# Kernel optimization log

Hardware: AMD Instinct MI355X
Metric: run time of the kernel (lower is better)

## Reference

```python
import jax, jax.numpy as jnp
import numpy as np

NS, NV = 48, 10
N_NODES, N_EDGES = 10000, 100000
N_EDGE_FEAT = 3 * NS  # 144
W_SS, W_VS, W_SV, W_VV = NS * NS, NV * NS, NS * NV, NV * NV
W_NUMEL = W_SS + W_VS + W_SV + W_VV  # 3364 = FullyConnectedTensorProduct.weight_numel
IN_DIM = NS + 3 * NV  # 78
EPS = 1e-5


def setup_inputs() -> dict:
    key = jax.random.key(0)
    ks = jax.random.split(key, 8)
    return {
        "node_attr": jax.random.normal(ks[0], (N_NODES, IN_DIM), jnp.float32),
        "edge_attr": jax.random.normal(ks[1], (N_EDGES, N_EDGE_FEAT), jnp.float32),
        "edge_sh": jax.random.normal(ks[2], (N_EDGES, 4), jnp.float32),
        "fc1_w": jax.random.normal(ks[3], (N_EDGE_FEAT, N_EDGE_FEAT), jnp.float32) / np.sqrt(N_EDGE_FEAT).astype(np.float32),
        "fc1_b": jnp.zeros((N_EDGE_FEAT,), jnp.float32),
        "fc2_w": jax.random.normal(ks[4], (N_EDGE_FEAT, W_NUMEL), jnp.float32) / np.sqrt(N_EDGE_FEAT).astype(np.float32),
        "fc2_b": jnp.zeros((W_NUMEL,), jnp.float32),
        "bn_weight": jnp.ones((NS + NV,), jnp.float32),
        "bn_bias": jnp.zeros((NS,), jnp.float32),
        "edge_index": jax.random.randint(ks[5], (2, N_EDGES), 0, N_NODES),
    }


def reference(node_attr, edge_attr, edge_sh, fc1_w, fc1_b, fc2_w, fc2_b, bn_weight, bn_bias, edge_index):
    edge_src, edge_dst = edge_index[0], edge_index[1]
    # --- gather node feats per edge, split into irreps ---
    x = node_attr[edge_dst]                      # [E, 78]
    xs = x[:, :NS]                               # [E, 48]  scalars (0e)
    xv = x[:, NS:].reshape(-1, NV, 3)            # [E, 10, 3] vectors (1o)
    s0 = edge_sh[:, 0]                           # [E]     sh 0e
    s1 = edge_sh[:, 1:4]                         # [E, 3]  sh 1o

    # --- per-edge TP weights from edge MLP ---
    w = jax.nn.relu(edge_attr @ fc1_w + fc1_b) @ fc2_w + fc2_b  # [E, 3364]
    w_ss = w[:, :W_SS].reshape(-1, NS, NS)
    w_vs = w[:, W_SS:W_SS + W_VS].reshape(-1, NV, NS)
    w_sv = w[:, W_SS + W_VS:W_SS + W_VS + W_SV].reshape(-1, NS, NV)
    w_vv = w[:, W_SS + W_VS + W_SV:].reshape(-1, NV, NV)

    # path normalization: 1/sqrt(mul_in * n_paths_into_output_irrep)
    a_ss = 1.0 / np.sqrt(NS * 2.0)
    a_vs = 1.0 / np.sqrt(NV * 2.0)
    a_sv = 1.0 / np.sqrt(NS * 2.0)
    a_vv = 1.0 / np.sqrt(NV * 2.0)

    # --- Clebsch-Gordan tensor product (fully connected, per-edge weights) ---
    # 0e (x) 0e -> 0e
    out_s = a_ss * jnp.einsum('ei,eio->eo', xs, w_ss) * s0[:, None]
    # 1o (x) 1o -> 0e  (CG = delta/sqrt(3))
    dot = jnp.einsum('eic,ec->ei', xv, s1) / np.sqrt(3.0)
    out_s = out_s + a_vs * jnp.einsum('ei,eio->eo', dot, w_vs)
    # 0e (x) 1o -> 1o
    out_v = a_sv * jnp.einsum('ei,eio->eo', xs, w_sv)[:, :, None] * s1[:, None, :]
    # 1o (x) 0e -> 1o
    out_v = out_v + a_vv * jnp.einsum('eic,eio->eoc', xv, w_vv) * s0[:, None, None]

    tp = jnp.concatenate([out_s, out_v.reshape(-1, 3 * NV)], axis=1)  # [E, 78]

    # --- scatter-mean to nodes ---
    sums = jax.ops.segment_sum(tp, edge_src, num_segments=N_NODES)
    cnt = jax.ops.segment_sum(jnp.ones((tp.shape[0],), tp.dtype), edge_src, num_segments=N_NODES)
    out = sums / jnp.maximum(cnt, 1.0)[:, None]

    # --- residual (in_dim == out_dim -> pad is a no-op) ---
    out = out + node_attr

    # --- equivariant batch norm (e3nn-style, batch statistics) ---
    os = out[:, :NS]
    ov = out[:, NS:].reshape(-1, NV, 3)
    mu = os.mean(0)
    var = os.var(0)
    os = (os - mu) / jnp.sqrt(var + EPS) * bn_weight[:NS] + bn_bias
    fn = (ov ** 2).sum(-1).mean(0) / 3.0  # component-normalized mean squared norm per channel
    ov = ov / jnp.sqrt(fn + EPS)[None, :, None] * bn_weight[NS:][None, :, None]
    return jnp.concatenate([os, ov.reshape(-1, 3 * NV)], axis=1)
```

## Files before the change

### kernel.cpp

```cpp
#include <hip/hip_runtime.h>
#include <hip/hip_bf16.h>

#define NS   48
#define NV   10
#define NEF  144
#define WN   3364
#define IND  78
#define NE   100000
#define NN   10000
#define EPS  1e-5f
#define HP   144

#define A_SS 0.10206207261596575f
#define A_VS 0.22360679774997896f
#define A_SV 0.10206207261596575f
#define A_VV 0.22360679774997896f
#define RS3  0.5773502691896258f

typedef __attribute__((ext_vector_type(8)))  short  short8;
typedef __attribute__((ext_vector_type(16))) float  f32x16;
typedef __attribute__((ext_vector_type(4)))  int    int4v;
typedef __attribute__((ext_vector_type(4)))  float  float4v;
typedef __attribute__((ext_vector_type(2)))  float  float2v;

#define MFMA32(a,b,c) __builtin_amdgcn_mfma_f32_32x32x16_bf16((a),(b),(c),0,0,0)

#define TP_F    0
#define ST_F    7800000
#define CNT_F   7800160
#define OFFS_F  7810160
#define CUR_F   7820164
#define EL_F    7830164
#define WSBF_F  7930168

#define OFF_W1  0
#define OFF_B1  23040
#define OFF_B2  468480
#define OFF_B3  561664
#define N_PREP  608256

__device__ __forceinline__ short tobf(float v) {
    return __builtin_bit_cast(short, __float2bfloat16(v));
}
__device__ __forceinline__ float fromb(short s) {
    unsigned u = ((unsigned)(unsigned short)s) << 16;
    return __builtin_bit_cast(float, u);
}
__device__ __forceinline__ unsigned pkt2(float a, float b) {
    unsigned ua = __builtin_bit_cast(unsigned, a);
    unsigned ub = __builtin_bit_cast(unsigned, b);
    return (ua >> 16) | (ub & 0xFFFF0000u);
}
__device__ __forceinline__ float waveReduceSum(float v) {
    #pragma unroll
    for (int o = 32; o > 0; o >>= 1) v += __shfl_down(v, o, 64);
    return v;
}

__global__ void prep_weights(const float* __restrict__ fc1_w,
                             const float* __restrict__ fc2_w,
                             const float* __restrict__ b2,
                             short* __restrict__ wsbf)
{
    int idx = blockIdx.x * 256 + threadIdx.x;
    if (idx >= N_PREP) return;
    float v = 0.f;
    if (idx < OFF_B1) {
        int r = idx;
        int tile = r / 4608, rem = r % 4608;
        int ks = rem / 512, l = (rem % 512) / 8, j = rem % 8;
        int n = tile * 32 + (l & 31);
        int k = ks * 16 + ((l >> 5) << 3) + j;
        v = (n < 144) ? fc1_w[k * 144 + n] : 0.f;
    } else if (idx < OFF_B2) {
        int r = idx - OFF_B1;
        if (r < 442368) {
            int i = r / 9216, rem = r % 9216;
            int tile = rem / 4608; rem %= 4608;
            int ks = rem / 512, l = (rem % 512) / 8, j = rem % 8;
            int n = tile * 32 + (l & 31);
            int k = ks * 16 + ((l >> 5) << 3) + j;
            if (n < 48)      v = fc2_w[(size_t)k * WN + i * 48 + n];
            else if (n < 58) v = fc2_w[(size_t)k * WN + 2784 + i * 10 + (n - 48)];
        } else {
            int rb = r - 442368;
            int tile = rb / 1536, rem = rb % 1536;
            int ks = rem / 512, l = (rem % 512) / 8, j = rem % 8;
            int n = tile * 32 + (l & 31);
            int k = ks * 16 + ((l >> 5) << 3) + j;
            if (n < 48)      v = b2[k * 48 + n];
            else if (n < 58) v = b2[2784 + k * 10 + (n - 48)];
        }
    } else if (idx < OFF_B3) {
        int r = idx - OFF_B2;
        if (r < 92160) {
            int i = r / 9216, rem = r % 9216;
            int tile = rem / 4608; rem %= 4608;
            int ks = rem / 512, l = (rem % 512) / 8, j = rem % 8;
            int n = tile * 32 + (l & 31);
            int k = ks * 16 + ((l >> 5) << 3) + j;
            if (n < 48) v = fc2_w[(size_t)k * WN + 2304 + i * 48 + n];
        } else {
            int rb = r - 92160;
            int tile = rb / 512, rem = rb % 512;
            int l = rem / 8, j = rem % 8;
            int n = tile * 32 + (l & 31);
            int k = ((l >> 5) << 3) + j;
            if (k < 10 && n < 48) v = b2[2304 + k * 48 + n];
        }
    } else {
        int r = idx - OFF_B3;
        if (r < 46080) {
            int i = r / 4608, rem = r % 4608;
            int ks = rem / 512, l = (rem % 512) / 8, j = rem % 8;
            int n = l & 31;
            int k = ks * 16 + ((l >> 5) << 3) + j;
            if (n < 10) v = fc2_w[(size_t)k * WN + 3264 + i * 10 + n];
        } else {
            int rb = r - 46080;
            int l = rb / 8, j = rb % 8;
            int n = l & 31;
            int k = ((l >> 5) << 3) + j;
            if (k < 10 && n < 10) v = b2[3264 + k * 10 + n];
        }
    }
    wsbf[idx] = tobf(v);
}

__global__ void hist_kernel(const int* __restrict__ eidx, int* __restrict__ cntI)
{
    int e = blockIdx.x * 256 + threadIdx.x;
    if (e < NE) atomicAdd(&cntI[eidx[e]], 1);
}

__global__ __launch_bounds__(1024) void scan_kernel(const int* __restrict__ cntI,
                                                    int* __restrict__ offs,
                                                    int* __restrict__ cursor)
{
    __shared__ int part[1024];
    int t = threadIdx.x;
    int base = t * 10;
    int local[10];
    int s = 0;
    #pragma unroll
    for (int q = 0; q < 10; ++q) {
        int i = base + q;
        int v = (i < NN) ? cntI[i] : 0;
        local[q] = s; s += v;
    }
    part[t] = s;
    __syncthreads();
    for (int o = 1; o < 1024; o <<= 1) {
        int v = (t >= o) ? part[t - o] : 0;
        __syncthreads();
        part[t] += v;
        __syncthreads();
    }
    int prev = (t == 0) ? 0 : part[t - 1];
    #pragma unroll
    for (int q = 0; q < 10; ++q) {
        int i = base + q;
        if (i < NN) { int val = prev + local[q]; offs[i] = val; cursor[i] = val; }
    }
    if (t == 1023) offs[NN] = part[1023];
}

__global__ void scatter_kernel(const int* __restrict__ eidx,
                               int* __restrict__ cursor, int* __restrict__ elist)
{
    int e = blockIdx.x * 256 + threadIdx.x;
    if (e < NE) {
        int pos = atomicAdd(&cursor[eidx[e]], 1);
        elist[pos] = e;
    }
}

__global__ __launch_bounds__(128, 2) void fused_main(
    const float* __restrict__ node_attr, const float* __restrict__ edge_attr,
    const float* __restrict__ edge_sh,   const float* __restrict__ b1,
    const int*   __restrict__ eidx,      const short* __restrict__ wsbf,
    float* __restrict__ tp)
{
    __shared__ short hlds[64 * HP];
    __shared__ short xfT[96 * 64];
    __shared__ float pbuf[64][10];
    __shared__ float s0s[64];
    __shared__ float s1s[64][3];

    const int t    = threadIdx.x;
    const int e0   = blockIdx.x * 64;
    const int lane = t & 63, wave = t >> 6;
    const int n32  = lane & 31, kh = lane >> 5;
    const int eL   = 32 * wave + n32;
    const int eLc  = min(e0 + eL, NE - 1);

    const short* W1L = wsbf + OFF_W1 + lane * 8;
    const short* B1L = wsbf + OFF_B1 + lane * 8;
    const short* B2L = wsbf + OFF_B2 + lane * 8;
    const short* B3L = wsbf + OFF_B3 + lane * 8;

    for (int idx = t; idx < 8 * 64; idx += 128) xfT[88 * 64 + idx] = 0;

    if (t < 64) {
        int ee = e0 + t;
        if (ee < NE) {
            float4v sh = *reinterpret_cast<const float4v*>(edge_sh + (size_t)ee * 4);
            s0s[t] = sh.x; s1s[t][0] = sh.y; s1s[t][1] = sh.z; s1s[t][2] = sh.w;
        } else {
            s0s[t] = 0.f; s1s[t][0] = s1s[t][1] = s1s[t][2] = 0.f;
        }
    }

    {
        const int eg  = t & 63;
        const int jb  = t >> 6;
        const int egc = min(e0 + eg, NE - 1);
        const int dst = eidx[NE + egc];
        const float* na = node_attr + (size_t)dst * IND;
        for (int j = jb; j < IND; j += 2) {
            int slot = (j < NS) ? j : 58 + ((j - NS) % 3) * 10 + (j - NS) / 3;
            xfT[slot * 64 + eg] = tobf(na[j]);
        }
    }

    short8 afc[9];
    {
        const float* ea = edge_attr + (size_t)eLc * NEF + kh * 8;
        #pragma unroll
        for (int ks = 0; ks < 9; ++ks) {
            float4v lo = *reinterpret_cast<const float4v*>(ea + ks * 16);
            float4v hi = *reinterpret_cast<const float4v*>(ea + ks * 16 + 4);
            int4v v = { (int)pkt2(lo.x, lo.y), (int)pkt2(lo.z, lo.w),
                        (int)pkt2(hi.x, hi.y), (int)pkt2(hi.z, hi.w) };
            afc[ks] = __builtin_bit_cast(short8, v);
        }
    }
    __syncthreads();

    #pragma unroll
    for (int it = 0; it < 5; ++it) {
        int e = t & 63;
        int i = (t >> 6) + 2 * it;
        float d = fromb(xfT[(58 + i) * 64 + e]) * s1s[e][0]
                + fromb(xfT[(68 + i) * 64 + e]) * s1s[e][1]
                + fromb(xfT[(78 + i) * 64 + e]) * s1s[e][2];
        xfT[(48 + i) * 64 + e] = tobf(d * RS3);
    }

    for (int pass = 0; pass < 3; ++pass) {
        int ntA = 2 * pass, ntB = 2 * pass + 1;
        bool hasB = (pass < 2);
        f32x16 accA = 0, accB = 0;
        #pragma unroll
        for (int ks = 0; ks < 9; ++ks) {
            short8 bA = *(const short8*)(W1L + (ntA * 9 + ks) * 512);
            accA = MFMA32(afc[ks], bA, accA);
            if (hasB) {
                short8 bB = *(const short8*)(W1L + (ntB * 9 + ks) * 512);
                accB = MFMA32(afc[ks], bB, accB);
            }
        }
        int colA = ntA * 32 + n32, colB = ntB * 32 + n32;
        float b1A = (colA < NEF) ? b1[colA] : 0.f;
        float b1B = (hasB && colB < NEF) ? b1[colB] : 0.f;
        #pragma unroll
        for (int r = 0; r < 16; ++r) {
            int row = (r & 3) + 8 * (r >> 2) + 4 * kh;
            int e = 32 * wave + row;
            if (colA < NEF) hlds[e * HP + colA] = tobf(fmaxf(accA[r] + b1A, 0.f));
            if (hasB)       hlds[e * HP + colB] = tobf(fmaxf(accB[r] + b1B, 0.f));
        }
    }
    __syncthreads();

    float2v hreg[36];
    #pragma unroll
    for (int ks = 0; ks < 9; ++ks) {
        int4v hh = *(const int4v*)(hlds + eL * HP + ks * 16 + kh * 8);
        #pragma unroll
        for (int q = 0; q < 4; ++q) {
            unsigned u = (unsigned)hh[q];
            float2v p;
            p.x = __builtin_bit_cast(float, u << 16);
            p.y = __builtin_bit_cast(float, u & 0xFFFF0000u);
            hreg[ks * 4 + q] = p;
        }
    }

    const int eoff = eL;

    f32x16 acc1a = 0, acc1b = 0, acc2a = 0, acc2b = 0;
    {
        #pragma unroll 1
        for (int i = 0; i < 48; ++i) {
            float xv = fromb(xfT[i * 64 + eoff]);
            float2v x2; x2.x = xv; x2.y = xv;
            const short* p0 = B1L + i * 9216;
            #pragma unroll
            for (int ks = 0; ks < 9; ++ks) {
                int4v v;
                #pragma unroll
                for (int q = 0; q < 4; ++q) {
                    float2v pr = hreg[ks * 4 + q] * x2;
                    v[q] = (int)pkt2(pr.x, pr.y);
                }
                short8 a  = __builtin_bit_cast(short8, v);
                short8 b0 = *(const short8*)(p0 + ks * 512);
                short8 b1f= *(const short8*)(p0 + 4608 + ks * 512);
                acc1a = MFMA32(a, b0, acc1a);
                acc1b = MFMA32(a, b1f, acc1b);
            }
        }
        #pragma unroll
        for (int ks = 0; ks < 3; ++ks) {
            short8 a;
            #pragma unroll
            for (int j = 0; j < 8; ++j)
                a[j] = xfT[(ks * 16 + kh * 8 + j) * 64 + eoff];
            short8 b0 = *(const short8*)(B1L + 442368 + ks * 512);
            short8 b1f= *(const short8*)(B1L + 442368 + 1536 + ks * 512);
            acc1a = MFMA32(a, b0, acc1a);
            acc1b = MFMA32(a, b1f, acc1b);
        }
    }
    {
        #pragma unroll 1
        for (int i = 0; i < 10; ++i) {
            float xv = fromb(xfT[(48 + i) * 64 + eoff]);
            float2v x2; x2.x = xv; x2.y = xv;
            const short* p0 = B2L + i * 9216;
            #pragma unroll
            for (int ks = 0; ks < 9; ++ks) {
                int4v v;
                #pragma unroll
                for (int q = 0; q < 4; ++q) {
                    float2v pr = hreg[ks * 4 + q] * x2;
                    v[q] = (int)pkt2(pr.x, pr.y);
                }
                short8 a  = __builtin_bit_cast(short8, v);
                short8 b0 = *(const short8*)(p0 + ks * 512);
                short8 b1f= *(const short8*)(p0 + 4608 + ks * 512);
                acc2a = MFMA32(a, b0, acc2a);
                acc2b = MFMA32(a, b1f, acc2b);
            }
        }
        {
            short8 a;
            #pragma unroll
            for (int j = 0; j < 8; ++j)
                a[j] = xfT[(48 + kh * 8 + j) * 64 + eoff];
            short8 b0 = *(const short8*)(B2L + 92160);
            short8 b1f= *(const short8*)(B2L + 92160 + 512);
            acc2a = MFMA32(a, b0, acc2a);
            acc2b = MFMA32(a, b1f, acc2b);
        }
    }
    #pragma unroll
    for (int r = 0; r < 16; ++r) {
        int row = (r & 3) + 8 * (r >> 2) + 4 * kh;
        int e = 32 * wave + row;
        int ge = e0 + e;
        if (ge < NE) {
            float s0e = s0s[e];
            float* rowp = tp + (size_t)ge * IND;
            rowp[n32] = A_SS * s0e * acc1a[r] + A_VS * acc2a[r];
            int col = 32 + n32;
            if (col < 48) {
                rowp[col] = A_SS * s0e * acc1b[r] + A_VS * acc2b[r];
            } else if (col < 58) {
                pbuf[e][col - 48] = A_SV * acc1b[r];
            }
        }
    }
    {
        #pragma unroll 1
        for (int c = 0; c < 3; ++c) {
            f32x16 acc3 = 0;
            #pragma unroll 1
            for (int i = 0; i < 10; ++i) {
                float xv = fromb(xfT[(58 + c * 10 + i) * 64 + eoff]);
                float2v x2; x2.x = xv; x2.y = xv;
                const short* p0 = B3L + i * 4608;
                #pragma unroll
                for (int ks = 0; ks < 9; ++ks) {
                    int4v v;
                    #pragma unroll
                    for (int q = 0; q < 4; ++q) {
                        float2v pr = hreg[ks * 4 + q] * x2;
                        v[q] = (int)pkt2(pr.x, pr.y);
                    }
                    short8 a  = __builtin_bit_cast(short8, v);
                    short8 b0 = *(const short8*)(p0 + ks * 512);
                    acc3 = MFMA32(a, b0, acc3);
                }
            }
            {
                short8 a;
                #pragma unroll
                for (int j = 0; j < 8; ++j)
                    a[j] = xfT[(58 + c * 10 + kh * 8 + j) * 64 + eoff];
                short8 b0 = *(const short8*)(B3L + 46080);
                acc3 = MFMA32(a, b0, acc3);
            }
            if (n32 < 10) {
                #pragma unroll
                for (int r = 0; r < 16; ++r) {
                    int row = (r & 3) + 8 * (r >> 2) + 4 * kh;
                    int e = 32 * wave + row;
                    int ge = e0 + e;
                    if (ge < NE) {
                        float p = pbuf[e][n32];
                        float q = A_VV * s0s[e] * acc3[r];
                        tp[(size_t)ge * IND + 48 + n32 * 3 + c] = p * s1s[e][c] + q;
                    }
                }
            }
        }
    }
}

__global__ __launch_bounds__(256) void gather_kernel(const float* __restrict__ tp,
                                                     const int* __restrict__ offs,
                                                     const int* __restrict__ elist,
                                                     const float* __restrict__ node_attr,
                                                     float* __restrict__ out)
{
    int node = blockIdx.x * 4 + (threadIdx.x >> 6);
    int lane = threadIdx.x & 63;
    if (node >= NN) return;
    int beg = offs[node], end = offs[node + 1];
    float a0 = 0.f, a1 = 0.f;
    for (int p = beg; p < end; ++p) {
        int e = elist[p];
        const float* row = tp + (size_t)e * IND;
        a0 += row[lane];
        if (lane < 14) a1 += row[64 + lane];
    }
    float c = fmaxf((float)(end - beg), 1.0f);
    size_t base = (size_t)node * IND;
    out[base + lane] = a0 / c + node_attr[base + lane];
    if (lane < 14) out[base + 64 + lane] = a1 / c + node_attr[base + 64 + lane];
}

__global__ __launch_bounds__(256) void stats_kernel(const float* __restrict__ pre,
                                                    const float* __restrict__ bnw,
                                                    float* __restrict__ stats)
{
    int j = blockIdx.x;
    int t = threadIdx.x;
    float s1 = 0.f, s2 = 0.f;
    if (j < NS) {
        for (int n = t; n < NN; n += 256) {
            float v = pre[(size_t)n * IND + j];
            s1 += v; s2 += v * v;
        }
    } else {
        int vch = j - NS;
        for (int n = t; n < NN; n += 256) {
            float a = pre[(size_t)n * IND + NS + vch * 3 + 0];
            float b = pre[(size_t)n * IND + NS + vch * 3 + 1];
            float d = pre[(size_t)n * IND + NS + vch * 3 + 2];
            s2 += a * a + b * b + d * d;
        }
    }
    __shared__ float r1[4], r2[4];
    s1 = waveReduceSum(s1);
    s2 = waveReduceSum(s2);
    int w = t >> 6, lane = t & 63;
    if (lane == 0) { r1[w] = s1; r2[w] = s2; }
    __syncthreads();
    if (t == 0) {
        float S1 = r1[0] + r1[1] + r1[2] + r1[3];
        float S2 = r2[0] + r2[1] + r2[2] + r2[3];
        if (j < NS) {
            float mu  = S1 / (float)NN;
            float var = S2 / (float)NN - mu * mu;
            stats[j]      = mu;
            stats[64 + j] = bnw[j] * rsqrtf(var + EPS);
        } else {
            int vch = j - NS;
            float fn = S2 / (3.0f * (float)NN);
            stats[128 + vch] = bnw[j] * rsqrtf(fn + EPS);
        }
    }
}

__global__ void normalize_kernel(const float* __restrict__ stats,
                                 const float* __restrict__ bnb,
                                 float* __restrict__ out)
{
    int idx = blockIdx.x * 256 + threadIdx.x;
    if (idx >= NN * IND) return;
    int j = idx % IND;
    float x = out[idx];
    if (j < NS) out[idx] = (x - stats[j]) * stats[64 + j] + bnb[j];
    else        out[idx] = x * stats[128 + (j - NS) / 3];
}

extern "C" void kernel_launch(void* const* d_in, const int* in_sizes, int n_in,
                              void* d_out, int out_size, void* d_ws, size_t ws_size,
                              hipStream_t stream)
{
    (void)in_sizes; (void)n_in; (void)out_size; (void)ws_size;
    const float* node_attr = (const float*)d_in[0];
    const float* edge_attr = (const float*)d_in[1];
    const float* edge_sh   = (const float*)d_in[2];
    const float* fc1_w     = (const float*)d_in[3];
    const float* fc1_b     = (const float*)d_in[4];
    const float* fc2_w     = (const float*)d_in[5];
    const float* fc2_b     = (const float*)d_in[6];
    const float* bn_w      = (const float*)d_in[7];
    const float* bn_b      = (const float*)d_in[8];
    const int*   eidx      = (const int*)d_in[9];

    float* wsf   = (float*)d_ws;
    float* tp    = wsf + TP_F;
    float* stats = wsf + ST_F;
    int*   cntI  = (int*)(wsf + CNT_F);
    int*   offs  = (int*)(wsf + OFFS_F);
    int*   cur   = (int*)(wsf + CUR_F);
    int*   elist = (int*)(wsf + EL_F);
    short* wsbf  = (short*)(wsf + WSBF_F);
    float* out   = (float*)d_out;

    (void)hipMemsetAsync(cntI, 0, NN * sizeof(int), stream);
    prep_weights<<<(N_PREP + 255) / 256, 256, 0, stream>>>(fc1_w, fc2_w, fc2_b, wsbf);
    hist_kernel<<<(NE + 255) / 256, 256, 0, stream>>>(eidx, cntI);
    scan_kernel<<<1, 1024, 0, stream>>>(cntI, offs, cur);
    scatter_kernel<<<(NE + 255) / 256, 256, 0, stream>>>(eidx, cur, elist);
    fused_main<<<(NE + 63) / 64, 128, 0, stream>>>(node_attr, edge_attr, edge_sh,
                                                   fc1_b, eidx, wsbf, tp);
    gather_kernel<<<(NN + 3) / 4, 256, 0, stream>>>(tp, offs, elist, node_attr, out);
    stats_kernel<<<NS + NV, 256, 0, stream>>>(out, bn_w, stats);
    normalize_kernel<<<(NN * IND + 255) / 256, 256, 0, stream>>>(stats, bn_b, out);
}
```

Baseline: 395.4 us.

## Double-buffer fc2 weight fragments in LDS and double edges per block

The main fused kernel now handles 128 edges per block with four waves instead of 64 with two. The fc2 weight fragments are streamed into a double-buffered LDS staging area with async global-to-LDS loads, so all waves share one copy instead of each fetching from global. The 1o×0e path also fuses its three component loops into one loop with three accumulators, reusing each B fragment. In exchange there is a block barrier every iteration and higher LDS and register pressure, which could reduce occupancy.

```diff
diff --git a/kernel.cpp b/kernel.cpp
--- a/kernel.cpp
+++ b/kernel.cpp
@@ -10,6 +10,7 @@
 #define NN   10000
 #define EPS  1e-5f
 #define HP   144
+#define EB   128
 
 #define A_SS 0.10206207261596575f
 #define A_VS 0.22360679774997896f
@@ -55,6 +56,11 @@
     #pragma unroll
     for (int o = 32; o > 0; o >>= 1) v += __shfl_down(v, o, 64);
     return v;
+}
+__device__ __forceinline__ void gl_lds16(const short* g, short* l) {
+    __builtin_amdgcn_global_load_lds(
+        (const __attribute__((address_space(1))) unsigned int*)g,
+        (__attribute__((address_space(3))) unsigned int*)l, 16, 0, 0);
 }
 
 __global__ void prep_weights(const float* __restrict__ fc1_w,
@@ -175,20 +181,20 @@
     }
 }
 
-__global__ __launch_bounds__(128, 2) void fused_main(
+__global__ __launch_bounds__(256, 2) void fused_main(
     const float* __restrict__ node_attr, const float* __restrict__ edge_attr,
     const float* __restrict__ edge_sh,   const float* __restrict__ b1,
     const int*   __restrict__ eidx,      const short* __restrict__ wsbf,
     float* __restrict__ tp)
 {
-    __shared__ short hlds[64 * HP];
-    __shared__ short xfT[96 * 64];
-    __shared__ float pbuf[64][10];
-    __shared__ float s0s[64];
-    __shared__ float s1s[64][3];
+    __shared__ short ubuf[18432];
+    __shared__ short xfT[96 * EB];
+    __shared__ float pbuf[EB][10];
+    __shared__ float s0s[EB];
+    __shared__ float s1s[EB][3];
 
     const int t    = threadIdx.x;
-    const int e0   = blockIdx.x * 64;
+    const int e0   = blockIdx.x * EB;
     const int lane = t & 63, wave = t >> 6;
     const int n32  = lane & 31, kh = lane >> 5;
     const int eL   = 32 * wave + n32;
@@ -199,9 +205,14 @@
     const short* B2L = wsbf + OFF_B2 + lane * 8;
     const short* B3L = wsbf + OFF_B3 + lane * 8;
 
-    for (int idx = t; idx < 8 * 64; idx += 128) xfT[88 * 64 + idx] = 0;
-
-    if (t < 64) {
+    auto stageB = [&](const short* src, short* dst, int nfrag) {
+        for (int f = wave; f < nfrag; f += 4)
+            gl_lds16(src + f * 512 + lane * 8, dst + f * 512);
+    };
+
+    for (int idx = t; idx < 8 * EB; idx += 256) xfT[88 * EB + idx] = 0;
+
+    if (t < EB) {
         int ee = e0 + t;
         if (ee < NE) {
             float4v sh = *reinterpret_cast<const float4v*>(edge_sh + (size_t)ee * 4);
@@ -212,14 +223,14 @@
     }
 
     {
-        const int eg  = t & 63;
-        const int jb  = t >> 6;
+        const int eg  = t & (EB - 1);
+        const int jb  = t >> 7;
         const int egc = min(e0 + eg, NE - 1);
         const int dst = eidx[NE + egc];
         const float* na = node_attr + (size_t)dst * IND;
         for (int j = jb; j < IND; j += 2) {
             int slot = (j < NS) ? j : 58 + ((j - NS) % 3) * 10 + (j - NS) / 3;
-            xfT[slot * 64 + eg] = tobf(na[j]);
+            xfT[slot * EB + eg] = tobf(na[j]);
         }
     }
 
@@ -239,12 +250,12 @@
 
     #pragma unroll
     for (int it = 0; it < 5; ++it) {
-        int e = t & 63;
-        int i = (t >> 6) + 2 * it;
-        float d = fromb(xfT[(58 + i) * 64 + e]) * s1s[e][0]
-                + fromb(xfT[(68 + i) * 64 + e]) * s1s[e][1]
-                + fromb(xfT[(78 + i) * 64 + e]) * s1s[e][2];
-        xfT[(48 + i) * 64 + e] = tobf(d * RS3);
+        int e = t & (EB - 1);
+        int i = (t >> 7) + 2 * it;
+        float d = fromb(xfT[(58 + i) * EB + e]) * s1s[e][0]
+                + fromb(xfT[(68 + i) * EB + e]) * s1s[e][1]
+                + fromb(xfT[(78 + i) * EB + e]) * s1s[e][2];
+        xfT[(48 + i) * EB + e] = tobf(d * RS3);
     }
 
     for (int pass = 0; pass < 3; ++pass) {
@@ -267,16 +278,15 @@
         for (int r = 0; r < 16; ++r) {
             int row = (r & 3) + 8 * (r >> 2) + 4 * kh;
             int e = 32 * wave + row;
-            if (colA < NEF) hlds[e * HP + colA] = tobf(fmaxf(accA[r] + b1A, 0.f));
-            if (hasB)       hlds[e * HP + colB] = tobf(fmaxf(accB[r] + b1B, 0.f));
-        }
-    }
-    __syncthreads();
+            if (colA < NEF) ubuf[e * HP + colA] = tobf(fmaxf(accA[r] + b1A, 0.f));
+            if (hasB)       ubuf[e * HP + colB] = tobf(fmaxf(accB[r] + b1B, 0.f));
+        }
+    }
 
     float2v hreg[36];
     #pragma unroll
     for (int ks = 0; ks < 9; ++ks) {
-        int4v hh = *(const int4v*)(hlds + eL * HP + ks * 16 + kh * 8);
+        int4v hh = *(const int4v*)(ubuf + eL * HP + ks * 16 + kh * 8);
         #pragma unroll
         for (int q = 0; q < 4; ++q) {
             unsigned u = (unsigned)hh[q];
@@ -286,37 +296,50 @@
             hreg[ks * 4 + q] = p;
         }
     }
-
-    const int eoff = eL;
+    __syncthreads();
+
+    short* stg0 = ubuf;
+    short* stg1 = ubuf + 9216;
+
+    stageB(wsbf + OFF_B1, stg0, 18);
+    __syncthreads();
+
+    auto genA = [&](float xv, int ks) -> short8 {
+        float2v x2; x2.x = xv; x2.y = xv;
+        int4v v;
+        #pragma unroll
+        for (int q = 0; q < 4; ++q) {
+            float2v pr = hreg[ks * 4 + q] * x2;
+            v[q] = (int)pkt2(pr.x, pr.y);
+        }
+        return __builtin_bit_cast(short8, v);
+    };
 
     f32x16 acc1a = 0, acc1b = 0, acc2a = 0, acc2b = 0;
     {
         #pragma unroll 1
         for (int i = 0; i < 48; ++i) {
-            float xv = fromb(xfT[i * 64 + eoff]);
-            float2v x2; x2.x = xv; x2.y = xv;
-            const short* p0 = B1L + i * 9216;
+            short* cur = (i & 1) ? stg1 : stg0;
+            short* nxt = (i & 1) ? stg0 : stg1;
+            if (i < 47) stageB(wsbf + OFF_B1 + (i + 1) * 9216, nxt, 18);
+            else        stageB(wsbf + OFF_B2, nxt, 18);
+            float xv = fromb(xfT[i * EB + eL]);
             #pragma unroll
             for (int ks = 0; ks < 9; ++ks) {
-                int4v v;
-                #pragma unroll
-                for (int q = 0; q < 4; ++q) {
-                    float2v pr = hreg[ks * 4 + q] * x2;
-                    v[q] = (int)pkt2(pr.x, pr.y);
-                }
-                short8 a  = __builtin_bit_cast(short8, v);
-                short8 b0 = *(const short8*)(p0 + ks * 512);
-                short8 b1f= *(const short8*)(p0 + 4608 + ks * 512);
+                short8 a  = genA(xv, ks);
+                short8 b0 = *(const short8*)(cur + ks * 512 + lane * 8);
+                short8 b1f= *(const short8*)(cur + 4608 + ks * 512 + lane * 8);
                 acc1a = MFMA32(a, b0, acc1a);
                 acc1b = MFMA32(a, b1f, acc1b);
             }
+            __syncthreads();
         }
         #pragma unroll
         for (int ks = 0; ks < 3; ++ks) {
             short8 a;
             #pragma unroll
             for (int j = 0; j < 8; ++j)
-                a[j] = xfT[(ks * 16 + kh * 8 + j) * 64 + eoff];
+                a[j] = xfT[(ks * 16 + kh * 8 + j) * EB + eL];
             short8 b0 = *(const short8*)(B1L + 442368 + ks * 512);
             short8 b1f= *(const short8*)(B1L + 442368 + 1536 + ks * 512);
             acc1a = MFMA32(a, b0, acc1a);
@@ -326,29 +349,26 @@
     {
         #pragma unroll 1
         for (int i = 0; i < 10; ++i) {
-            float xv = fromb(xfT[(48 + i) * 64 + eoff]);
-            float2v x2; x2.x = xv; x2.y = xv;
-            const short* p0 = B2L + i * 9216;
+            short* cur = (i & 1) ? stg1 : stg0;
+            short* nxt = (i & 1) ? stg0 : stg1;
+            if (i < 9) stageB(wsbf + OFF_B2 + (i + 1) * 9216, nxt, 18);
+            else       stageB(wsbf + OFF_B3, nxt, 9);
+            float xv = fromb(xfT[(48 + i) * EB + eL]);
             #pragma unroll
             for (int ks = 0; ks < 9; ++ks) {
-                int4v v;
-                #pragma unroll
-                for (int q = 0; q < 4; ++q) {
-                    float2v pr = hreg[ks * 4 + q] * x2;
-                    v[q] = (int)pkt2(pr.x, pr.y);
-                }
-                short8 a  = __builtin_bit_cast(short8, v);
-                short8 b0 = *(const short8*)(p0 + ks * 512);
-                short8 b1f= *(const short8*)(p0 + 4608 + ks * 512);
+                short8 a  = genA(xv, ks);
+                short8 b0 = *(const short8*)(cur + ks * 512 + lane * 8);
+                short8 b1f= *(const short8*)(cur + 4608 + ks * 512 + lane * 8);
                 acc2a = MFMA32(a, b0, acc2a);
                 acc2b = MFMA32(a, b1f, acc2b);
             }
+            __syncthreads();
         }
         {
             short8 a;
             #pragma unroll
             for (int j = 0; j < 8; ++j)
-                a[j] = xfT[(48 + kh * 8 + j) * 64 + eoff];
+                a[j] = xfT[(48 + kh * 8 + j) * EB + eL];
             short8 b0 = *(const short8*)(B2L + 92160);
             short8 b1f= *(const short8*)(B2L + 92160 + 512);
             acc2a = MFMA32(a, b0, acc2a);
@@ -373,46 +393,50 @@
         }
     }
     {
+        f32x16 acc30 = 0, acc31 = 0, acc32 = 0;
         #pragma unroll 1
-        for (int c = 0; c < 3; ++c) {
-            f32x16 acc3 = 0;
-            #pragma unroll 1
-            for (int i = 0; i < 10; ++i) {
-                float xv = fromb(xfT[(58 + c * 10 + i) * 64 + eoff]);
-                float2v x2; x2.x = xv; x2.y = xv;
-                const short* p0 = B3L + i * 4608;
-                #pragma unroll
-                for (int ks = 0; ks < 9; ++ks) {
-                    int4v v;
-                    #pragma unroll
-                    for (int q = 0; q < 4; ++q) {
-                        float2v pr = hreg[ks * 4 + q] * x2;
-                        v[q] = (int)pkt2(pr.x, pr.y);
-                    }
-                    short8 a  = __builtin_bit_cast(short8, v);
-                    short8 b0 = *(const short8*)(p0 + ks * 512);
-                    acc3 = MFMA32(a, b0, acc3);
-                }
+        for (int i = 0; i < 10; ++i) {
+            short* cur = (i & 1) ? stg1 : stg0;
+            short* nxt = (i & 1) ? stg0 : stg1;
+            if (i < 9) stageB(wsbf + OFF_B3 + (i + 1) * 4608, nxt, 9);
+            float xv0 = fromb(xfT[(58 + i) * EB + eL]);
+            float xv1 = fromb(xfT[(68 + i) * EB + eL]);
+            float xv2 = fromb(xfT[(78 + i) * EB + eL]);
+            #pragma unroll
+            for (int ks = 0; ks < 9; ++ks) {
+                short8 b0 = *(const short8*)(cur + ks * 512 + lane * 8);
+                acc30 = MFMA32(genA(xv0, ks), b0, acc30);
+                acc31 = MFMA32(genA(xv1, ks), b0, acc31);
+                acc32 = MFMA32(genA(xv2, ks), b0, acc32);
             }
-            {
-                short8 a;
-                #pragma unroll
-                for (int j = 0; j < 8; ++j)
-                    a[j] = xfT[(58 + c * 10 + kh * 8 + j) * 64 + eoff];
-                short8 b0 = *(const short8*)(B3L + 46080);
-                acc3 = MFMA32(a, b0, acc3);
-            }
-            if (n32 < 10) {
-                #pragma unroll
-                for (int r = 0; r < 16; ++r) {
-                    int row = (r & 3) + 8 * (r >> 2) + 4 * kh;
-                    int e = 32 * wave + row;
-                    int ge = e0 + e;
-                    if (ge < NE) {
-                        float p = pbuf[e][n32];
-                        float q = A_VV * s0s[e] * acc3[r];
-                        tp[(size_t)ge * IND + 48 + n32 * 3 + c] = p * s1s[e][c] + q;
-                    }
+            __syncthreads();
+        }
+        {
+            short8 bb = *(const short8*)(B3L + 46080);
+            short8 a;
+            #pragma unroll
+            for (int j = 0; j < 8; ++j) a[j] = xfT[(58 + kh * 8 + j) * EB + eL];
+            acc30 = MFMA32(a, bb, acc30);
+            #pragma unroll
+            for (int j = 0; j < 8; ++j) a[j] = xfT[(68 + kh * 8 + j) * EB + eL];
+            acc31 = MFMA32(a, bb, acc31);
+            #pragma unroll
+            for (int j = 0; j < 8; ++j) a[j] = xfT[(78 + kh * 8 + j) * EB + eL];
+            acc32 = MFMA32(a, bb, acc32);
+        }
+        if (n32 < 10) {
+            #pragma unroll
+            for (int r = 0; r < 16; ++r) {
+                int row = (r & 3) + 8 * (r >> 2) + 4 * kh;
+                int e = 32 * wave + row;
+                int ge = e0 + e;
+                if (ge < NE) {
+                    float p  = pbuf[e][n32];
+                    float qs = A_VV * s0s[e];
+                    size_t base = (size_t)ge * IND + 48 + n32 * 3;
+                    tp[base + 0] = p * s1s[e][0] + qs * acc30[r];
+                    tp[base + 1] = p * s1s[e][1] + qs * acc31[r];
+                    tp[base + 2] = p * s1s[e][2] + qs * acc32[r];
                 }
             }
         }
@@ -528,8 +552,8 @@
     hist_kernel<<<(NE + 255) / 256, 256, 0, stream>>>(eidx, cntI);
     scan_kernel<<<1, 1024, 0, stream>>>(cntI, offs, cur);
     scatter_kernel<<<(NE + 255) / 256, 256, 0, stream>>>(eidx, cur, elist);
-    fused_main<<<(NE + 63) / 64, 128, 0, stream>>>(node_attr, edge_attr, edge_sh,
-                                                   fc1_b, eidx, wsbf, tp);
+    fused_main<<<(NE + EB - 1) / EB, 256, 0, stream>>>(node_attr, edge_attr, edge_sh,
+                                                       fc1_b, eidx, wsbf, tp);
     gather_kernel<<<(NN + 3) / 4, 256, 0, stream>>>(tp, offs, elist, node_attr, out);
     stats_kernel<<<NS + NV, 256, 0, stream>>>(out, bn_w, stats);
     normalize_kernel<<<(NN * IND + 255) / 256, 256, 0, stream>>>(stats, bn_b, out);
```

After: 378.8 us. 4.2% less time.
